# Optimization experiments

Measured on AMD Instinct MI355X. Metric: run time of the kernel, lower is better.

## Reference

```python
import jax, jax.numpy as jnp
import numpy as np

T = 0.1      # CosKernel temperature
EPS = 1e-6   # CosKernel norm epsilon
SCALE = 10.0 # logit scale applied after max-subtract


def setup_inputs() -> dict:
    key = jax.random.key(0)
    k1, k2 = jax.random.split(key)
    b, d, h, w = 8, 512, 40, 40
    fs_1 = jax.random.normal(k1, (b, d, h, w), dtype=jnp.float32)
    fs_2 = jax.random.normal(k2, (b, d, h, w), dtype=jnp.float32)
    return {"fs_1": fs_1, "fs_2": fs_2}


def reference(fs_1, fs_2):
    b, d, h, w = fs_1.shape
    N = h * w
    # rearrange 'b d h w -> b (h w) d'
    x = fs_1.reshape(b, d, N).transpose(0, 2, 1)  # [b, N, d]
    y = fs_2.reshape(b, d, N).transpose(0, 2, 1)  # [b, N, d]
    # CosKernel: exp((cos_sim - 1) / T)
    dots = jnp.einsum("bnd,bmd->bnm", x, y)
    norms = (jnp.linalg.norm(x, axis=-1)[:, :, None]
             * jnp.linalg.norm(y, axis=-1)[:, None, :] + EPS)
    c = dots / norms                          # [b, N, M] cosine similarity
    K = jnp.exp((c - 1.0) / T)                # [b, N, M]
    # view(b,h,w,-1).permute(0,3,1,2) -> channel dim = target index M
    distances = K.reshape(b, h, w, N).transpose(0, 3, 1, 2)  # [b, M, h, w]
    max_vals = jnp.max(distances, axis=1, keepdims=True)      # [b, 1, h, w]
    gm_cls = (distances - max_vals) * SCALE                   # [b, M, h, w]
    # cls_to_flow (deterministic): grid of target coords, gather at argmax
    res = round(float(np.sqrt(N)))  # == h == w
    lin = jnp.linspace(-1.0 + 1.0 / res, 1.0 - 1.0 / res, res, dtype=jnp.float32)
    Gy, Gx = jnp.meshgrid(lin, lin, indexing="ij")
    G = jnp.stack([Gx, Gy], axis=-1).reshape(N, 2)            # [M, 2] (x, y)
    idx = jnp.argmax(gm_cls, axis=1)                          # [b, h, w]
    flow = G[idx].transpose(0, 3, 1, 2)                       # [b, 2, h, w]
    gm_certainty = jnp.max(gm_cls, axis=1, keepdims=True)     # [b, 1, h, w]
    return gm_cls, gm_certainty, flow
```

## Files before the change

kernel.cpp:

```cpp
#include <hip/hip_runtime.h>
#include <math.h>

#define B 8
#define D 512
#define N 1600
#define NP 1664
#define NRES 40

static constexpr float EPS_K   = 1e-6f;
static constexpr float INV_T   = 10.0f;
static constexpr float SCALE_K = 10.0f;
static constexpr float BAND    = 0.99f;
static constexpr float L2E10   = 14.4269504089f;

using f32x4 = __attribute__((ext_vector_type(4))) float;
using h8    = __attribute__((ext_vector_type(8))) _Float16;
using u16x4 = __attribute__((ext_vector_type(4))) unsigned short;

__device__ __forceinline__ void gload16(const void* g, void* l) {
    __builtin_amdgcn_global_load_lds(
        (const __attribute__((address_space(1))) void*)g,
        (__attribute__((address_space(3))) void*)l, 16, 0, 0);
}

__global__ __launch_bounds__(256)
void split_transpose_kernel(const float* __restrict__ f1, const float* __restrict__ f2,
                            short* __restrict__ Xh, short* __restrict__ Yh,
                            float* __restrict__ Xf, float* __restrict__ Yf,
                            float* __restrict__ partial) {
    int bx = blockIdx.x;
    int by = blockIdx.y;
    int bz = blockIdx.z;
    int b = bz & 7, which = bz >> 3;
    const float* src = which ? f2 : f1;
    short* oh = which ? Yh : Xh;
    float* of = which ? Yf : Xf;

    __shared__ float Ts[64][65];
    __shared__ float red[64][17];
    int t = threadIdx.x;
    int n0 = bx * 64, d0 = by * 64;
    bool valid = (n0 < N);
    int c4 = (t & 15) * 4, g16 = t >> 4;

    #pragma unroll
    for (int p = 0; p < 4; ++p) {
        int dl = g16 + p * 16;
        float4 v = make_float4(0.f, 0.f, 0.f, 0.f);
        if (valid) v = *(const float4*)&src[((size_t)b * D + d0 + dl) * N + n0 + c4];
        Ts[dl][c4 + 0] = v.x; Ts[dl][c4 + 1] = v.y;
        Ts[dl][c4 + 2] = v.z; Ts[dl][c4 + 3] = v.w;
    }
    __syncthreads();
    #pragma unroll
    for (int p = 0; p < 4; ++p) {
        int nl = g16 + p * 16;
        float vv[4];
        unsigned int hw[2];
        float ssp = 0.f;
        #pragma unroll
        for (int q = 0; q < 2; ++q) {
            unsigned int wv = 0;
            #pragma unroll
            for (int i = 0; i < 2; ++i) {
                float v = Ts[c4 + q * 2 + i][nl];
                vv[q * 2 + i] = v;
                ssp = fmaf(v, v, ssp);
                _Float16 h = (_Float16)v;
                unsigned short hb = __builtin_bit_cast(unsigned short, h);
                wv |= ((unsigned int)hb) << (16 * i);
            }
            hw[q] = wv;
        }
        red[nl][c4 >> 2] = ssp;
        size_t o = ((size_t)b * NP + n0 + nl) * D + d0 + c4;
        *(uint2*)&oh[o] = make_uint2(hw[0], hw[1]);
        *(float4*)&of[o] = make_float4(vv[0], vv[1], vv[2], vv[3]);
    }
    __syncthreads();
    if (t < 64) {
        float s = 0.f;
        #pragma unroll
        for (int g = 0; g < 16; ++g) s += red[t][g];
        partial[(((size_t)which * 8 + b) * 8 + by) * NP + n0 + t] = s;
    }
}

__global__ __launch_bounds__(256)
void norms_reduce_kernel(const float* __restrict__ partial,
                         float* __restrict__ norm1, float* __restrict__ norm2) {
    int id = blockIdx.x * 256 + threadIdx.x;
    if (id >= 2 * B * N) return;
    int which = id / (B * N);
    int r = id % (B * N);
    int b = r / N, n = r % N;
    float s = 0.f;
    #pragma unroll
    for (int dt = 0; dt < 8; ++dt)
        s += partial[(((size_t)which * 8 + b) * 8 + dt) * NP + n];
    (which ? norm2 : norm1)[b * N + n] = sqrtf(s);
}

__global__ __launch_bounds__(256)
void norms_kernel(const float* __restrict__ fs1, const float* __restrict__ fs2,
                  float* __restrict__ norm1, float* __restrict__ norm2) {
    int bid   = blockIdx.x;
    int ntile = bid % 25;
    int b     = (bid / 25) % B;
    int which = bid / (25 * B);
    const float* src = which ? fs2 : fs1;
    float*       dst = which ? norm2 : norm1;

    int t = threadIdx.x, nl = t & 63, doff = t >> 6;
    int n = ntile * 64 + nl;
    const float* base = src + (size_t)b * D * N + n;
    float acc = 0.f;
    for (int d = doff; d < D; d += 4) {
        float v = base[(size_t)d * N];
        acc = fmaf(v, v, acc);
    }
    __shared__ float red[4][64];
    red[doff][nl] = acc;
    __syncthreads();
    if (t < 64) {
        float s = red[0][t] + red[1][t] + red[2][t] + red[3][t];
        dst[b * N + ntile * 64 + t] = sqrtf(s);
    }
}

__device__ __forceinline__ h8 ldfragh(const short* tile, int row, int l) {
    int s = ((l >> 4) ^ (row >> 1)) & 3;
    return *(const h8*)(tile + row * 32 + s * 8);
}

template<bool USE_KH>
__global__ __launch_bounds__(256, 4)
void gemm_fp16_kernel(const short* __restrict__ Yh, const short* __restrict__ Xh,
                      const float* __restrict__ norm1, const float* __restrict__ norm2,
                      unsigned int* __restrict__ mx, float* __restrict__ out,
                      unsigned short* __restrict__ Kh) {
    __shared__ short lds[2][8192];

    int lin = blockIdx.x;
    int b    = lin & 7;
    int rem  = lin >> 3;
    int mblk = rem % 13;
    int nblk = rem / 13;
    int m0 = mblk * 128, n0 = nblk * 128;

    int t = threadIdx.x, l = t & 63, w = t >> 6;
    int mwoff = (w & 1) * 64;
    int nwoff = (w >> 1) * 64;
    size_t bNP = (size_t)b * NP;
    int l15 = l & 15;

    const short* gp[4];
    int lo[4];
    #pragma unroll
    for (int j = 0; j < 4; ++j) {
        int q = w * 4 + j;
        int tile = q >> 3, rg = q & 7;
        int row  = rg * 16 + (l >> 2);
        int slotg = (l & 3) ^ ((row >> 1) & 3);
        const short* base = tile ? Xh : Yh;
        int rows0 = tile ? n0 : m0;
        gp[j] = base + (bNP + rows0 + row) * (size_t)D + slotg * 8;
        lo[j] = tile * 4096 + rg * 512;
    }

    #define ST(nb)                                             \
    {   _Pragma("unroll")                                      \
        for (int j = 0; j < 4; ++j) {                          \
            gload16(gp[j], &lds[nb][lo[j]]);                   \
            gp[j] += 32;                                       \
        }                                                      \
    }

    f32x4 acc[4][4];
    #pragma unroll
    for (int i = 0; i < 4; i++)
        #pragma unroll
        for (int j = 0; j < 4; j++) acc[i][j] = (f32x4)0.f;

    ST(0);

    for (int tt = 0; tt < 16; ++tt) {
        int cur = tt & 1;
        if (tt < 15) {
            ST(cur ^ 1);
            asm volatile("s_waitcnt vmcnt(4)" ::: "memory");
        } else {
            asm volatile("s_waitcnt vmcnt(0)" ::: "memory");
        }
        __builtin_amdgcn_s_barrier();
        asm volatile("" ::: "memory");

        const short* Ah = &lds[cur][0];
        const short* Bh = &lds[cur][4096];

        h8 bh[4];
        #pragma unroll
        for (int nj = 0; nj < 4; ++nj)
            bh[nj] = ldfragh(Bh, nwoff + nj * 16 + l15, l);
        __builtin_amdgcn_s_setprio(1);
        #pragma unroll
        for (int mi = 0; mi < 4; ++mi) {
            h8 ah = ldfragh(Ah, mwoff + mi * 16 + l15, l);
            #pragma unroll
            for (int nj = 0; nj < 4; ++nj)
                acc[mi][nj] = __builtin_amdgcn_mfma_f32_16x16x32_f16(ah, bh[nj], acc[mi][nj], 0, 0, 0);
        }
        __builtin_amdgcn_s_setprio(0);
        asm volatile("s_waitcnt lgkmcnt(0)" ::: "memory");
        __builtin_amdgcn_s_barrier();
    }
    #undef ST

    int hi4 = l >> 4;
    float rn1v[4];
    int   ng[4];
    #pragma unroll
    for (int nj = 0; nj < 4; ++nj) {
        ng[nj]  = n0 + nwoff + nj * 16 + l15;
        float n1 = (ng[nj] < N) ? norm1[b * N + ng[nj]] : 1.f;
        rn1v[nj] = __builtin_amdgcn_rcpf(n1);
    }
    float pmax[4] = {0.f, 0.f, 0.f, 0.f};
    size_t obase = (size_t)b * N * N;

    #pragma unroll
    for (int mi = 0; mi < 4; ++mi) {
        #pragma unroll
        for (int r = 0; r < 4; ++r) {
            int mg = m0 + mwoff + mi * 16 + hi4 * 4 + r;
            bool mok = (mg < N);
            float rn2 = mok ? __builtin_amdgcn_rcpf(norm2[b * N + mg]) : 1.f;
            #pragma unroll
            for (int nj = 0; nj < 4; ++nj) {
                float c = acc[mi][nj][r] * rn2 * rn1v[nj];
                float k = exp2f((c - 1.f) * L2E10);
                if (!mok) k = 0.f;
                if constexpr (USE_KH) {
                    _Float16 h = (_Float16)k;
                    float kr = (float)h;
                    pmax[nj] = fmaxf(pmax[nj], kr);
                    if (mok && ng[nj] < N)
                        Kh[obase + (size_t)mg * N + ng[nj]] = __builtin_bit_cast(unsigned short, h);
                } else {
                    pmax[nj] = fmaxf(pmax[nj], k);
                    if (mok && ng[nj] < N)
                        out[obase + (size_t)mg * N + ng[nj]] = k;
                }
            }
        }
    }
    #pragma unroll
    for (int nj = 0; nj < 4; ++nj) {
        float v = pmax[nj];
        v = fmaxf(v, __shfl_xor(v, 16, 64));
        v = fmaxf(v, __shfl_xor(v, 32, 64));
        if (hi4 == 0 && ng[nj] < N)
            atomicMax(&mx[b * N + ng[nj]], __float_as_uint(v));
    }
}

#define BK 16
#define BT 128
__global__ __launch_bounds__(256)
void gemm_exp_kernel(const float* __restrict__ fs1, const float* __restrict__ fs2,
                     const float* __restrict__ norm1, const float* __restrict__ norm2,
                     unsigned int* __restrict__ mx, float* __restrict__ out) {
    int m0 = blockIdx.x * BT, n0 = blockIdx.y * BT, b = blockIdx.z;
    int t = threadIdx.x, tx = t & 15, ty = t >> 4;
    __shared__ float Xs[BK][BT];
    __shared__ float Ys[BK][BT];
    __shared__ float red[BT][17];
    const float* Xb = fs1 + (size_t)b * D * N;
    const float* Yb = fs2 + (size_t)b * D * N;
    float acc[8][8];
    #pragma unroll
    for (int i = 0; i < 8; i++)
        #pragma unroll
        for (int j = 0; j < 8; j++) acc[i][j] = 0.f;
    int r0 = t >> 5, c4 = (t & 31) * 4;
    bool xok = (n0 + c4) < N, yok = (m0 + c4) < N;
    for (int kk = 0; kk < D; kk += BK) {
        #pragma unroll
        for (int rr = 0; rr < 2; rr++) {
            int r = r0 + rr * 8, d = kk + r;
            float4 xv = make_float4(0, 0, 0, 0), yv = make_float4(0, 0, 0, 0);
            if (xok) xv = *(const float4*)&Xb[(size_t)d * N + n0 + c4];
            if (yok) yv = *(const float4*)&Yb[(size_t)d * N + m0 + c4];
            *(float4*)&Xs[r][c4] = xv;
            *(float4*)&Ys[r][c4] = yv;
        }
        __syncthreads();
        #pragma unroll
        for (int d = 0; d < BK; d++) {
            float4 a0 = *(const float4*)&Xs[d][ty * 4];
            float4 a1 = *(const float4*)&Xs[d][64 + ty * 4];
            float4 b0 = *(const float4*)&Ys[d][tx * 4];
            float4 b1 = *(const float4*)&Ys[d][64 + tx * 4];
            float av[8] = {a0.x, a0.y, a0.z, a0.w, a1.x, a1.y, a1.z, a1.w};
            float bv[8] = {b0.x, b0.y, b0.z, b0.w, b1.x, b1.y, b1.z, b1.w};
            #pragma unroll
            for (int i = 0; i < 8; i++)
                #pragma unroll
                for (int j = 0; j < 8; j++)
                    acc[i][j] = fmaf(av[i], bv[j], acc[i][j]);
        }
        __syncthreads();
    }
    int ng[8], mg[8];
    float n1v[8], n2v[8];
    #pragma unroll
    for (int q = 0; q < 8; q++) {
        ng[q] = n0 + ((q < 4) ? (ty * 4 + q) : (64 + ty * 4 + q - 4));
        mg[q] = m0 + ((q < 4) ? (tx * 4 + q) : (64 + tx * 4 + q - 4));
        n1v[q] = (ng[q] < N) ? norm1[b * N + ng[q]] : 1.f;
        n2v[q] = (mg[q] < N) ? norm2[b * N + mg[q]] : 1.f;
    }
    float pmax[8];
    #pragma unroll
    for (int i = 0; i < 8; i++) pmax[i] = 0.f;
    size_t obase = (size_t)b * N * N;
    #pragma unroll
    for (int j = 0; j < 8; j++) {
        float kcol[8];
        #pragma unroll
        for (int i = 0; i < 8; i++) {
            float c = acc[i][j] / (n1v[i] * n2v[j] + EPS_K);
            float k = expf((c - 1.f) * INV_T);
            if (mg[j] >= N) k = 0.f;
            kcol[i] = k;
            pmax[i] = fmaxf(pmax[i], k);
        }
        if (mg[j] < N) {
            size_t rowb = obase + (size_t)mg[j] * N;
            float4 v0 = {kcol[0], kcol[1], kcol[2], kcol[3]};
            *(float4*)&out[rowb + ng[0]] = v0;
            if (ng[4] < N) {
                float4 v1 = {kcol[4], kcol[5], kcol[6], kcol[7]};
                *(float4*)&out[rowb + ng[4]] = v1;
            }
        }
    }
    #pragma unroll
    for (int q = 0; q < 8; q++) {
        int nloc = (q < 4) ? (ty * 4 + q) : (64 + ty * 4 + q - 4);
        red[nloc][tx] = pmax[q];
    }
    __syncthreads();
    if (t < BT) {
        float mval = red[t][0];
        #pragma unroll
        for (int x = 1; x < 16; x++) mval = fmaxf(mval, red[t][x]);
        int n = n0 + t;
        if (n < N) atomicMax(&mx[b * N + n], __float_as_uint(mval));
    }
}

__global__ __launch_bounds__(256)
void fix_argmax_f16_kernel(const unsigned short* __restrict__ Kh, float* __restrict__ out,
                           const unsigned int* __restrict__ mx, int* __restrict__ bestm,
                           unsigned int* __restrict__ candCount, int* __restrict__ candM) {
    int nt = blockIdx.x;
    int mq = blockIdx.y;
    int b  = blockIdx.z;
    int t  = threadIdx.x;
    int n0 = nt * 256 + (t & 63) * 4;
    int moff = t >> 6;
    if (n0 >= N) return;

    float4 mxv = *(const float4*)&((const float*)mx)[b * N + n0];
    float4 th  = make_float4(mxv.x * BAND, mxv.y * BAND, mxv.z * BAND, mxv.w * BAND);
    size_t base = (size_t)b * N * N + n0;
    int mend = mq * 50 + 50;
    for (int m = mq * 50 + moff; m < mend; m += 4) {
        size_t idx = base + (size_t)m * N;
        u16x4 kv = *(const u16x4*)&Kh[idx];
        float k0 = (float)__builtin_bit_cast(_Float16, (unsigned short)kv[0]);
        float k1 = (float)__builtin_bit_cast(_Float16, (unsigned short)kv[1]);
        float k2 = (float)__builtin_bit_cast(_Float16, (unsigned short)kv[2]);
        float k3 = (float)__builtin_bit_cast(_Float16, (unsigned short)kv[3]);
        float4 o;
        o.x = (k0 - mxv.x) * SCALE_K;
        o.y = (k1 - mxv.y) * SCALE_K;
        o.z = (k2 - mxv.z) * SCALE_K;
        o.w = (k3 - mxv.w) * SCALE_K;
        *(float4*)&out[idx] = o;
        #pragma unroll
        for (int j = 0; j < 4; ++j) {
            float vv = (j == 0) ? k0 : (j == 1) ? k1 : (j == 2) ? k2 : k3;
            float tt = (j == 0) ? th.x : (j == 1) ? th.y : (j == 2) ? th.z : th.w;
            if (vv >= tt) {
                int pix = b * N + n0 + j;
                unsigned int slot = atomicAdd(&candCount[pix], 1u);
                if (slot < 15) candM[pix * 16 + slot] = m;
                atomicMin(&bestm[pix], m);
            }
        }
    }
}

__global__ __launch_bounds__(256)
void fix_argmax_kernel(float* __restrict__ out, const unsigned int* __restrict__ mx,
                       int* __restrict__ bestm, unsigned int* __restrict__ candCount,
                       int* __restrict__ candM) {
    int nt = blockIdx.x;
    int mq = blockIdx.y;
    int b  = blockIdx.z;
    int t  = threadIdx.x;
    int n0 = nt * 256 + (t & 63) * 4;
    int moff = t >> 6;
    if (n0 >= N) return;

    float4 mxv = *(const float4*)&((const float*)mx)[b * N + n0];
    float4 th  = make_float4(mxv.x * BAND, mxv.y * BAND, mxv.z * BAND, mxv.w * BAND);
    size_t base = (size_t)b * N * N + n0;
    int mend = mq * 50 + 50;
    for (int m = mq * 50 + moff; m < mend; m += 4) {
        size_t idx = base + (size_t)m * N;
        float4 v = *(float4*)&out[idx];
        float4 o;
        o.x = (v.x - mxv.x) * SCALE_K;
        o.y = (v.y - mxv.y) * SCALE_K;
        o.z = (v.z - mxv.z) * SCALE_K;
        o.w = (v.w - mxv.w) * SCALE_K;
        *(float4*)&out[idx] = o;
        #pragma unroll
        for (int j = 0; j < 4; ++j) {
            float vv = (j == 0) ? v.x : (j == 1) ? v.y : (j == 2) ? v.z : v.w;
            float tt = (j == 0) ? th.x : (j == 1) ? th.y : (j == 2) ? th.z : th.w;
            if (vv >= tt) {
                int pix = b * N + n0 + j;
                unsigned int slot = atomicAdd(&candCount[pix], 1u);
                if (slot < 15) candM[pix * 16 + slot] = m;
                atomicMin(&bestm[pix], m);
            }
        }
    }
}

__global__ __launch_bounds__(256)
void refine_kernel(const float* __restrict__ Xf, const float* __restrict__ Yf,
                   const float* __restrict__ norm1, const float* __restrict__ norm2,
                   const unsigned int* __restrict__ candCount, const int* __restrict__ candM,
                   int* __restrict__ bestm) {
    int nwaves = (gridDim.x * 256) >> 6;
    int wv = (blockIdx.x * 256 + threadIdx.x) >> 6;
    int l  = threadIdx.x & 63;
    for (int pix = wv; pix < B * N; pix += nwaves) {
        unsigned int cnt = candCount[pix];
        if (cnt < 2) continue;
        int b = pix / N, n = pix % N;
        const float* p1 = Xf + ((size_t)b * NP + n) * D;
        float n1 = norm1[pix];
        float bestc = -2.f;
        int   bi = N;
        int ncand = (cnt <= 15) ? (int)cnt : N;
        for (int e = 0; e < ncand; ++e) {
            int m = (cnt <= 15) ? candM[pix * 16 + e] : e;
            const float* p2 = Yf + ((size_t)b * NP + m) * D;
            float acc = 0.f;
            #pragma unroll
            for (int q = 0; q < 2; ++q) {
                float4 a = *(const float4*)&p1[l * 8 + q * 4];
                float4 c = *(const float4*)&p2[l * 8 + q * 4];
                acc = fmaf(a.x, c.x, acc);
                acc = fmaf(a.y, c.y, acc);
                acc = fmaf(a.z, c.z, acc);
                acc = fmaf(a.w, c.w, acc);
            }
            #pragma unroll
            for (int off = 1; off < 64; off <<= 1)
                acc += __shfl_xor(acc, off, 64);
            float cc = acc / (n1 * norm2[b * N + m] + EPS_K);
            if (cc > bestc || (cc == bestc && m < bi)) { bestc = cc; bi = m; }
        }
        if (l == 0) bestm[pix] = bi;
    }
}

__global__ __launch_bounds__(256)
void refine_fb_kernel(const float* __restrict__ fs1, const float* __restrict__ fs2,
                      const float* __restrict__ norm1, const float* __restrict__ norm2,
                      const unsigned int* __restrict__ mx, const unsigned int* __restrict__ candCount,
                      int* __restrict__ bestm, const float* __restrict__ out) {
    int nwaves = (gridDim.x * 256) >> 6;
    int wv = (blockIdx.x * 256 + threadIdx.x) >> 6;
    int l  = threadIdx.x & 63;
    for (int pix = wv; pix < B * N; pix += nwaves) {
        if (candCount[pix] < 2) continue;
        int b = pix / N, n = pix % N;
        float mxv = __uint_as_float(mx[pix]);
        float gth = -(1.f - BAND) * SCALE_K * mxv;
        const float* col = out + (size_t)b * N * N + n;
        const float* p1  = fs1 + (size_t)b * D * N + n;
        float n1 = norm1[pix];
        float bestc = -2.f;
        int   bi = 0;
        for (int it = 0; it < 25; ++it) {
            int m = it * 64 + l;
            float g = col[(size_t)m * N];
            unsigned long long mask = __ballot(g >= gth);
            while (mask) {
                int s = __ffsll(mask) - 1;
                mask &= mask - 1;
                int mc = it * 64 + s;
                const float* p2 = fs2 + (size_t)b * D * N + mc;
                float acc = 0.f;
                #pragma unroll
                for (int d8 = 0; d8 < 8; ++d8) {
                    int d = d8 * 64 + l;
                    acc = fmaf(p1[(size_t)d * N], p2[(size_t)d * N], acc);
                }
                #pragma unroll
                for (int off = 1; off < 64; off <<= 1)
                    acc += __shfl_xor(acc, off, 64);
                float cc = acc / (n1 * norm2[b * N + mc] + EPS_K);
                if (cc > bestc) { bestc = cc; bi = mc; }
            }
        }
        if (l == 0) bestm[pix] = bi;
    }
}

__global__ __launch_bounds__(256)
void flow_kernel(float* __restrict__ out, const int* __restrict__ bestm) {
    int id = blockIdx.x * 256 + threadIdx.x;
    if (id >= B * N) return;
    int b = id / N, n = id % N;
    int bm = bestm[id];
    int i = bm / NRES, j = bm % NRES;
    const float step = 1.95f / 39.f;
    float gx = fmaf(step, (float)j, -0.975f);
    float gy = fmaf(step, (float)i, -0.975f);
    const size_t CERT_OFF = (size_t)B * N * N;
    const size_t FLOW_OFF = CERT_OFF + (size_t)B * N;
    out[CERT_OFF + id] = 0.f;
    out[FLOW_OFF + (size_t)(b * 2) * N + n]     = gx;
    out[FLOW_OFF + (size_t)(b * 2 + 1) * N + n] = gy;
}

extern "C" void kernel_launch(void* const* d_in, const int* in_sizes, int n_in,
                              void* d_out, int out_size, void* d_ws, size_t ws_size,
                              hipStream_t stream) {
    const float* fs1 = (const float*)d_in[0];
    const float* fs2 = (const float*)d_in[1];
    float* out = (float*)d_out;

    const size_t SPLIT = (size_t)B * NP * D;
    const size_t SMALL = 5 * (size_t)B * N * 4 + 16 * (size_t)B * N * 4 + 64;
    const size_t NEED_MID  = 2 * SPLIT * sizeof(short)
                           + 2 * SPLIT * sizeof(float)
                           + SMALL;
    const size_t NEED_FULL = NEED_MID + (size_t)B * N * N * sizeof(unsigned short);

    if (ws_size >= NEED_MID) {
        bool full = (ws_size >= NEED_FULL);
        short* Yh = (short*)d_ws;
        short* Xh = Yh + SPLIT;
        float* Yf = (float*)(Xh + SPLIT);
        float* Xf = Yf + SPLIT;
        unsigned short* Kh = (unsigned short*)(Xf + SPLIT);
        char* tail = (char*)(Kh + (full ? (size_t)B * N * N : 0));
        float* norm1 = (float*)tail;
        float* norm2 = norm1 + B * N;
        unsigned int* mx = (unsigned int*)(norm2 + B * N);
        int* bestm = (int*)(mx + B * N);
        unsigned int* candCount = (unsigned int*)(bestm + B * N);
        int* candM = (int*)(candCount + B * N);
        float* partial = out;

        hipMemsetAsync(mx, 0, B * N * sizeof(unsigned int), stream);
        hipMemsetAsync(bestm, 0x7f, B * N * sizeof(int), stream);
        hipMemsetAsync(candCount, 0, B * N * sizeof(unsigned int), stream);

        split_transpose_kernel<<<dim3(26, 8, 16), 256, 0, stream>>>(
            fs1, fs2, Xh, Yh, Xf, Yf, partial);
        norms_reduce_kernel<<<dim3(100), 256, 0, stream>>>(partial, norm1, norm2);
        if (full) {
            gemm_fp16_kernel<true><<<dim3(1352), 256, 0, stream>>>(Yh, Xh, norm1, norm2,
                                                                   mx, out, Kh);
            fix_argmax_f16_kernel<<<dim3(7, 32, B), 256, 0, stream>>>(Kh, out, mx, bestm,
                                                                      candCount, candM);
        } else {
            gemm_fp16_kernel<false><<<dim3(1352), 256, 0, stream>>>(Yh, Xh, norm1, norm2,
                                                                    mx, out, nullptr);
            fix_argmax_kernel<<<dim3(7, 32, B), 256, 0, stream>>>(out, mx, bestm,
                                                                  candCount, candM);
        }
        refine_kernel<<<dim3(320), 256, 0, stream>>>(Xf, Yf, norm1, norm2,
                                                     candCount, candM, bestm);
        flow_kernel<<<dim3((B * N + 255) / 256), 256, 0, stream>>>(out, bestm);
    } else {
        float* norm1 = (float*)d_ws;
        float* norm2 = norm1 + B * N;
        unsigned int* mx = (unsigned int*)(norm2 + B * N);
        int* bestm = (int*)(mx + B * N);
        unsigned int* candCount = (unsigned int*)(bestm + B * N);
        int* candM = (int*)(candCount + B * N);

        hipMemsetAsync(mx, 0, B * N * sizeof(unsigned int), stream);
        hipMemsetAsync(bestm, 0x7f, B * N * sizeof(int), stream);
        hipMemsetAsync(candCount, 0, B * N * sizeof(unsigned int), stream);

        norms_kernel<<<dim3(2 * B * 25), 256, 0, stream>>>(fs1, fs2, norm1, norm2);
        gemm_exp_kernel<<<dim3(13, 13, B), 256, 0, stream>>>(fs1, fs2, norm1, norm2, mx, out);
        fix_argmax_kernel<<<dim3(7, 32, B), 256, 0, stream>>>(out, mx, bestm,
                                                              candCount, candM);
        refine_fb_kernel<<<dim3(320), 256, 0, stream>>>(fs1, fs2, norm1, norm2,
                                                        mx, candCount, bestm, out);
        flow_kernel<<<dim3((B * N + 255) / 256), 256, 0, stream>>>(out, bestm);
    }
}
```

Measured before the change: 114.7 us.

## Fuse fp16 GEMM and argmax-fix pass via a grid-wide barrier

Replaces the fp16 GEMM launch and the separate fix_argmax pass with one persistent-style kernel. Each block computes two M-tiles for a fixed N-tile, waits on a global atomic counter until all 728 blocks finish, then normalises its own region of Kh into the output and records argmax candidates. This saves a kernel launch and tail gap and improves locality for the Kh reread. In exchange it relies on all 728 blocks being co-resident, which holds only if occupancy allows it; otherwise the bounded spin times out and the results can be wrong.

```diff
diff --git a/kernel.cpp b/kernel.cpp
--- a/kernel.cpp
+++ b/kernel.cpp
@@ -6,6 +6,7 @@
 #define N 1600
 #define NP 1664
 #define NRES 40
+#define FUSED_GRID 728
 
 static constexpr float EPS_K   = 1e-6f;
 static constexpr float INV_T   = 10.0f;
@@ -133,21 +134,200 @@
     return *(const h8*)(tile + row * 32 + s * 8);
 }
 
-template<bool USE_KH>
+__global__ __launch_bounds__(256, 4)
+void gemm_fused_kernel(const short* __restrict__ Yh, const short* __restrict__ Xh,
+                       const float* __restrict__ norm1, const float* __restrict__ norm2,
+                       unsigned int* __restrict__ mx, unsigned short* __restrict__ Kh,
+                       float* __restrict__ out, int* __restrict__ bestm,
+                       unsigned int* __restrict__ candCount, int* __restrict__ candM,
+                       unsigned int* __restrict__ ctr) {
+    __shared__ short lds[2][8192];
+
+    int lin = blockIdx.x;
+    int b    = lin & 7;
+    int rem  = lin >> 3;
+    int mp   = rem % 7;
+    int nblk = rem / 7;
+    int n0 = nblk * 128;
+
+    int t = threadIdx.x, l = t & 63, w = t >> 6;
+    int mwoff = (w & 1) * 64;
+    int nwoff = (w >> 1) * 64;
+    size_t bNP = (size_t)b * NP;
+    int l15 = l & 15;
+    size_t obase = (size_t)b * N * N;
+
+    for (int sub = 0; sub < 2; ++sub) {
+        int mblk = mp * 2 + sub;
+        if (mblk > 12) break;
+        int m0 = mblk * 128;
+
+        const short* gp[4];
+        int lo[4];
+        #pragma unroll
+        for (int j = 0; j < 4; ++j) {
+            int q = w * 4 + j;
+            int tile = q >> 3, rg = q & 7;
+            int row  = rg * 16 + (l >> 2);
+            int slotg = (l & 3) ^ ((row >> 1) & 3);
+            const short* base = tile ? Xh : Yh;
+            int rows0 = tile ? n0 : m0;
+            gp[j] = base + (bNP + rows0 + row) * (size_t)D + slotg * 8;
+            lo[j] = tile * 4096 + rg * 512;
+        }
+
+        #define ST(nb)                                             \
+        {   _Pragma("unroll")                                      \
+            for (int j = 0; j < 4; ++j) {                          \
+                gload16(gp[j], &lds[nb][lo[j]]);                   \
+                gp[j] += 32;                                       \
+            }                                                      \
+        }
+
+        f32x4 acc[4][4];
+        #pragma unroll
+        for (int i = 0; i < 4; i++)
+            #pragma unroll
+            for (int j = 0; j < 4; j++) acc[i][j] = (f32x4)0.f;
+
+        ST(0);
+
+        for (int tt = 0; tt < 16; ++tt) {
+            int cur = tt & 1;
+            if (tt < 15) {
+                ST(cur ^ 1);
+                asm volatile("s_waitcnt vmcnt(4)" ::: "memory");
+            } else {
+                asm volatile("s_waitcnt vmcnt(0)" ::: "memory");
+            }
+            __builtin_amdgcn_s_barrier();
+            asm volatile("" ::: "memory");
+
+            const short* Ah = &lds[cur][0];
+            const short* Bh = &lds[cur][4096];
+
+            h8 bh[4];
+            #pragma unroll
+            for (int nj = 0; nj < 4; ++nj)
+                bh[nj] = ldfragh(Bh, nwoff + nj * 16 + l15, l);
+            __builtin_amdgcn_s_setprio(1);
+            #pragma unroll
+            for (int mi = 0; mi < 4; ++mi) {
+                h8 ah = ldfragh(Ah, mwoff + mi * 16 + l15, l);
+                #pragma unroll
+                for (int nj = 0; nj < 4; ++nj)
+                    acc[mi][nj] = __builtin_amdgcn_mfma_f32_16x16x32_f16(ah, bh[nj], acc[mi][nj], 0, 0, 0);
+            }
+            __builtin_amdgcn_s_setprio(0);
+            asm volatile("s_waitcnt lgkmcnt(0)" ::: "memory");
+            __builtin_amdgcn_s_barrier();
+        }
+        #undef ST
+
+        int hi4 = l >> 4;
+        float rn1v[4];
+        int   ng[4];
+        #pragma unroll
+        for (int nj = 0; nj < 4; ++nj) {
+            ng[nj]  = n0 + nwoff + nj * 16 + l15;
+            float n1 = (ng[nj] < N) ? norm1[b * N + ng[nj]] : 1.f;
+            rn1v[nj] = __builtin_amdgcn_rcpf(n1);
+        }
+        float pmax[4] = {0.f, 0.f, 0.f, 0.f};
+
+        #pragma unroll
+        for (int mi = 0; mi < 4; ++mi) {
+            #pragma unroll
+            for (int r = 0; r < 4; ++r) {
+                int mg = m0 + mwoff + mi * 16 + hi4 * 4 + r;
+                bool mok = (mg < N);
+                float rn2 = mok ? __builtin_amdgcn_rcpf(norm2[b * N + mg]) : 1.f;
+                #pragma unroll
+                for (int nj = 0; nj < 4; ++nj) {
+                    float c = acc[mi][nj][r] * rn2 * rn1v[nj];
+                    float k = exp2f((c - 1.f) * L2E10);
+                    if (!mok) k = 0.f;
+                    _Float16 h = (_Float16)k;
+                    float kr = (float)h;
+                    pmax[nj] = fmaxf(pmax[nj], kr);
+                    if (mok && ng[nj] < N)
+                        Kh[obase + (size_t)mg * N + ng[nj]] = __builtin_bit_cast(unsigned short, h);
+                }
+            }
+        }
+        #pragma unroll
+        for (int nj = 0; nj < 4; ++nj) {
+            float v = pmax[nj];
+            v = fmaxf(v, __shfl_xor(v, 16, 64));
+            v = fmaxf(v, __shfl_xor(v, 32, 64));
+            if (hi4 == 0 && ng[nj] < N)
+                atomicMax(&mx[b * N + ng[nj]], __float_as_uint(v));
+        }
+        __syncthreads();
+    }
+
+    __syncthreads();
+    if (t == 0) {
+        __hip_atomic_fetch_add(ctr, 1u, __ATOMIC_RELEASE, __HIP_MEMORY_SCOPE_AGENT);
+        int spins = 0;
+        while (__hip_atomic_load(ctr, __ATOMIC_ACQUIRE, __HIP_MEMORY_SCOPE_AGENT) < (unsigned)FUSED_GRID) {
+            __builtin_amdgcn_s_sleep(16);
+            if (++spins > (1 << 22)) break;
+        }
+    }
+    __syncthreads();
+
+    int tn = t & 31, tm = t >> 5;
+    int nc = n0 + tn * 4;
+    if (nc < N) {
+        float mxv[4], th[4];
+        #pragma unroll
+        for (int j = 0; j < 4; ++j) {
+            unsigned int u = __hip_atomic_load(&mx[b * N + nc + j],
+                                               __ATOMIC_ACQUIRE, __HIP_MEMORY_SCOPE_AGENT);
+            mxv[j] = __uint_as_float(u);
+            th[j]  = mxv[j] * BAND;
+        }
+        int mstart = mp * 256;
+        int mend   = mstart + 256; if (mend > N) mend = N;
+        for (int m = mstart + tm; m < mend; m += 8) {
+            size_t idx = obase + (size_t)m * N + nc;
+            u16x4 kv = *(const u16x4*)&Kh[idx];
+            float k0 = (float)__builtin_bit_cast(_Float16, (unsigned short)kv[0]);
+            float k1 = (float)__builtin_bit_cast(_Float16, (unsigned short)kv[1]);
+            float k2 = (float)__builtin_bit_cast(_Float16, (unsigned short)kv[2]);
+            float k3 = (float)__builtin_bit_cast(_Float16, (unsigned short)kv[3]);
+            float4 o;
+            o.x = (k0 - mxv[0]) * SCALE_K;
+            o.y = (k1 - mxv[1]) * SCALE_K;
+            o.z = (k2 - mxv[2]) * SCALE_K;
+            o.w = (k3 - mxv[3]) * SCALE_K;
+            *(float4*)&out[idx] = o;
+            #pragma unroll
+            for (int j = 0; j < 4; ++j) {
+                float vv = (j == 0) ? k0 : (j == 1) ? k1 : (j == 2) ? k2 : k3;
+                if (vv >= th[j]) {
+                    int pix = b * N + nc + j;
+                    unsigned int slot = atomicAdd(&candCount[pix], 1u);
+                    if (slot < 15) candM[pix * 16 + slot] = m;
+                    atomicMin(&bestm[pix], m);
+                }
+            }
+        }
+    }
+}
+
 __global__ __launch_bounds__(256, 4)
 void gemm_fp16_kernel(const short* __restrict__ Yh, const short* __restrict__ Xh,
                       const float* __restrict__ norm1, const float* __restrict__ norm2,
-                      unsigned int* __restrict__ mx, float* __restrict__ out,
-                      unsigned short* __restrict__ Kh) {
+                      unsigned int* __restrict__ mx, float* __restrict__ out) {
     __shared__ short lds[2][8192];
-
     int lin = blockIdx.x;
     int b    = lin & 7;
     int rem  = lin >> 3;
     int mblk = rem % 13;
     int nblk = rem / 13;
     int m0 = mblk * 128, n0 = nblk * 128;
-
     int t = threadIdx.x, l = t & 63, w = t >> 6;
     int mwoff = (w & 1) * 64;
     int nwoff = (w >> 1) * 64;
@@ -167,7 +347,6 @@
         gp[j] = base + (bNP + rows0 + row) * (size_t)D + slotg * 8;
         lo[j] = tile * 4096 + rg * 512;
     }
-
     #define ST(nb)                                             \
     {   _Pragma("unroll")                                      \
         for (int j = 0; j < 4; ++j) {                          \
@@ -175,15 +354,12 @@
             gp[j] += 32;                                       \
         }                                                      \
     }
-
     f32x4 acc[4][4];
     #pragma unroll
     for (int i = 0; i < 4; i++)
         #pragma unroll
         for (int j = 0; j < 4; j++) acc[i][j] = (f32x4)0.f;
-
     ST(0);
-
     for (int tt = 0; tt < 16; ++tt) {
         int cur = tt & 1;
         if (tt < 15) {
@@ -194,10 +370,8 @@
         }
         __builtin_amdgcn_s_barrier();
         asm volatile("" ::: "memory");
-
         const short* Ah = &lds[cur][0];
         const short* Bh = &lds[cur][4096];
-
         h8 bh[4];
         #pragma unroll
         for (int nj = 0; nj < 4; ++nj)
@@ -215,7 +389,6 @@
         __builtin_amdgcn_s_barrier();
     }
     #undef ST
-
     int hi4 = l >> 4;
     float rn1v[4];
     int   ng[4];
@@ -227,7 +400,6 @@
     }
     float pmax[4] = {0.f, 0.f, 0.f, 0.f};
     size_t obase = (size_t)b * N * N;
-
     #pragma unroll
     for (int mi = 0; mi < 4; ++mi) {
         #pragma unroll
@@ -240,17 +412,9 @@
                 float c = acc[mi][nj][r] * rn2 * rn1v[nj];
                 float k = exp2f((c - 1.f) * L2E10);
                 if (!mok) k = 0.f;
-                if constexpr (USE_KH) {
-                    _Float16 h = (_Float16)k;
-                    float kr = (float)h;
-                    pmax[nj] = fmaxf(pmax[nj], kr);
-                    if (mok && ng[nj] < N)
-                        Kh[obase + (size_t)mg * N + ng[nj]] = __builtin_bit_cast(unsigned short, h);
-                } else {
-                    pmax[nj] = fmaxf(pmax[nj], k);
-                    if (mok && ng[nj] < N)
-                        out[obase + (size_t)mg * N + ng[nj]] = k;
-                }
+                pmax[nj] = fmaxf(pmax[nj], k);
+                if (mok && ng[nj] < N)
+                    out[obase + (size_t)mg * N + ng[nj]] = k;
             }
         }
     }
@@ -357,49 +521,6 @@
         for (int x = 1; x < 16; x++) mval = fmaxf(mval, red[t][x]);
         int n = n0 + t;
         if (n < N) atomicMax(&mx[b * N + n], __float_as_uint(mval));
-    }
-}
-
-__global__ __launch_bounds__(256)
-void fix_argmax_f16_kernel(const unsigned short* __restrict__ Kh, float* __restrict__ out,
-                           const unsigned int* __restrict__ mx, int* __restrict__ bestm,
-                           unsigned int* __restrict__ candCount, int* __restrict__ candM) {
-    int nt = blockIdx.x;
-    int mq = blockIdx.y;
-    int b  = blockIdx.z;
-    int t  = threadIdx.x;
-    int n0 = nt * 256 + (t & 63) * 4;
-    int moff = t >> 6;
-    if (n0 >= N) return;
-
-    float4 mxv = *(const float4*)&((const float*)mx)[b * N + n0];
-    float4 th  = make_float4(mxv.x * BAND, mxv.y * BAND, mxv.z * BAND, mxv.w * BAND);
-    size_t base = (size_t)b * N * N + n0;
-    int mend = mq * 50 + 50;
-    for (int m = mq * 50 + moff; m < mend; m += 4) {
-        size_t idx = base + (size_t)m * N;
-        u16x4 kv = *(const u16x4*)&Kh[idx];
-        float k0 = (float)__builtin_bit_cast(_Float16, (unsigned short)kv[0]);
-        float k1 = (float)__builtin_bit_cast(_Float16, (unsigned short)kv[1]);
-        float k2 = (float)__builtin_bit_cast(_Float16, (unsigned short)kv[2]);
-        float k3 = (float)__builtin_bit_cast(_Float16, (unsigned short)kv[3]);
-        float4 o;
-        o.x = (k0 - mxv.x) * SCALE_K;
-        o.y = (k1 - mxv.y) * SCALE_K;
-        o.z = (k2 - mxv.z) * SCALE_K;
-        o.w = (k3 - mxv.w) * SCALE_K;
-        *(float4*)&out[idx] = o;
-        #pragma unroll
-        for (int j = 0; j < 4; ++j) {
-            float vv = (j == 0) ? k0 : (j == 1) ? k1 : (j == 2) ? k2 : k3;
-            float tt = (j == 0) ? th.x : (j == 1) ? th.y : (j == 2) ? th.z : th.w;
-            if (vv >= tt) {
-                int pix = b * N + n0 + j;
-                unsigned int slot = atomicAdd(&candCount[pix], 1u);
-                if (slot < 15) candM[pix * 16 + slot] = m;
-                atomicMin(&bestm[pix], m);
-            }
-        }
     }
 }
 
@@ -551,7 +672,7 @@
     float* out = (float*)d_out;
 
     const size_t SPLIT = (size_t)B * NP * D;
-    const size_t SMALL = 5 * (size_t)B * N * 4 + 16 * (size_t)B * N * 4 + 64;
+    const size_t SMALL = 5 * (size_t)B * N * 4 + 16 * (size_t)B * N * 4 + 256;
     const size_t NEED_MID  = 2 * SPLIT * sizeof(short)
                            + 2 * SPLIT * sizeof(float)
                            + SMALL;
@@ -571,23 +692,22 @@
         int* bestm = (int*)(mx + B * N);
         unsigned int* candCount = (unsigned int*)(bestm + B * N);
         int* candM = (int*)(candCount + B * N);
+        unsigned int* ctr = (unsigned int*)(candM + 16 * B * N);
         float* partial = out;
 
         hipMemsetAsync(mx, 0, B * N * sizeof(unsigned int), stream);
         hipMemsetAsync(bestm, 0x7f, B * N * sizeof(int), stream);
         hipMemsetAsync(candCount, 0, B * N * sizeof(unsigned int), stream);
+        hipMemsetAsync(ctr, 0, 64, stream);
 
         split_transpose_kernel<<<dim3(26, 8, 16), 256, 0, stream>>>(
             fs1, fs2, Xh, Yh, Xf, Yf, partial);
         norms_reduce_kernel<<<dim3(100), 256, 0, stream>>>(partial, norm1, norm2);
         if (full) {
-            gemm_fp16_kernel<true><<<dim3(1352), 256, 0, stream>>>(Yh, Xh, norm1, norm2,
-                                                                   mx, out, Kh);
-            fix_argmax_f16_kernel<<<dim3(7, 32, B), 256, 0, stream>>>(Kh, out, mx, bestm,
-                                                                      candCount, candM);
+            gemm_fused_kernel<<<dim3(FUSED_GRID), 256, 0, stream>>>(
+                Yh, Xh, norm1, norm2, mx, Kh, out, bestm, candCount, candM, ctr);
         } else {
-            gemm_fp16_kernel<false><<<dim3(1352), 256, 0, stream>>>(Yh, Xh, norm1, norm2,
-                                                                    mx, out, nullptr);
+            gemm_fp16_kernel<<<dim3(1352), 256, 0, stream>>>(Yh, Xh, norm1, norm2, mx, out);
             fix_argmax_kernel<<<dim3(7, 32, B), 256, 0, stream>>>(out, mx, bestm,
                                                                   candCount, candM);
         }
```

New measurement: 388.2 us. 3.38x slower.
